# Kernel optimization log

Measured on AMD Instinct MI355X. Metric: run time of the kernel, lower is better.

Reference implementation:

```python
import jax, jax.numpy as jnp
import numpy as np

B, T, HIDDEN, CQ, CKV, NH, HD, RD = 4, 4096, 4096, 1536, 512, 32, 128, 64


def _rope(x):
    # x: (b, s, n, r); positions = arange(s) (decode step gets pos 0, matching
    # the module which passes no offset to RotaryPositionEmbedding)
    s, r = x.shape[1], x.shape[-1]
    inv_freq = 1.0 / (10000.0 ** (jnp.arange(0, r, 2, dtype=jnp.float32) / r))
    ang = jnp.arange(s, dtype=jnp.float32)[:, None] * inv_freq[None, :]  # (s, r/2)
    cos = jnp.cos(ang)[None, :, None, :].astype(x.dtype)
    sin = jnp.sin(ang)[None, :, None, :].astype(x.dtype)
    x1, x2 = x[..., ::2], x[..., 1::2]
    return jnp.stack([x1 * cos - x2 * sin, x1 * sin + x2 * cos], axis=-1).reshape(x.shape)


def setup_inputs() -> dict:
    key = jax.random.key(0)
    ks = jax.random.split(key, 12)
    wscale = jnp.float32(0.02)
    return {
        "hidden_states": jax.random.normal(ks[0], (B, 1, HIDDEN), jnp.float32),
        "mask": jnp.zeros((B, 1, NH, T + 1), jnp.float32),
        "cached_cKV": jax.random.normal(ks[1], (B, T, CKV), jnp.float32),
        "cached_kR": jax.random.normal(ks[2], (B, T, NH, RD), jnp.float32),
        "W_DQ": jax.random.normal(ks[3], (HIDDEN, CQ), jnp.float32) * wscale,
        "W_DKV": jax.random.normal(ks[4], (HIDDEN, CKV), jnp.float32) * wscale,
        "W_UQ_C": jax.random.normal(ks[5], (CQ, NH, HD), jnp.float32) * wscale,
        "W_UQ_R": jax.random.normal(ks[6], (CQ, NH, RD), jnp.float32) * wscale,
        "W_UK_C": jax.random.normal(ks[7], (CKV, NH, HD), jnp.float32) * wscale,
        "W_UV_C": jax.random.normal(ks[8], (CKV, NH, HD), jnp.float32) * wscale,
        "W_KR": jax.random.normal(ks[9], (HIDDEN, NH, RD), jnp.float32) * wscale,
        "W_O": jax.random.normal(ks[10], (NH, HD, HIDDEN), jnp.float32) * wscale,
    }


def reference(hidden_states, mask, cached_cKV, cached_kR,
              W_DQ, W_DKV, W_UQ_C, W_UQ_R, W_UK_C, W_UV_C, W_KR, W_O):
    Bc = hidden_states.shape[0]
    # query path
    cQ_t = jnp.einsum('bsh,hq->bsq', hidden_states, W_DQ)
    qC_t = jnp.einsum('bsq,qnd->bsnd', cQ_t, W_UQ_C)
    qR_t = jnp.einsum('bsq,qnr->bsnr', cQ_t, W_UQ_R)
    kR_t_raw = jnp.einsum('bsh,hnr->bsnr', hidden_states, W_KR)
    qR_t = _rope(qR_t)
    kR_t = _rope(kR_t_raw)
    # compressed KV for the new token
    cKV_t = jnp.einsum('bsh,hv->bsv', hidden_states, W_DKV)
    kC_t = jnp.einsum('bsv,vnd->bsnd', cKV_t, W_UK_C)
    vC_t = jnp.einsum('bsv,vnd->bsnd', cKV_t, W_UV_C)
    # decompress prefix cache and score
    prefix_len = cached_cKV.shape[1]
    kC_prefix = jnp.einsum('btv,vnd->btnd', cached_cKV, W_UK_C)   # (B,T,n,d)
    prefix_scores = (jnp.einsum('bsnd,btnd->bsnt', qC_t, kC_prefix)
                     + jnp.einsum('bsnr,btnr->bsnt', qR_t, cached_kR))
    new_score = (jnp.einsum('bsnd,bsnd->bsn', qC_t, kC_t)
                 + jnp.einsum('bsnr,bsnr->bsn', qR_t, kR_t))[..., None]
    attn_scores = jnp.concatenate([prefix_scores, new_score], axis=-1)
    scale = jnp.sqrt(jnp.float32(HD + RD)).astype(attn_scores.dtype)
    attn_scores = attn_scores / scale
    if mask is not None:
        attn_scores = attn_scores + mask * jnp.asarray(-1e9, attn_scores.dtype)
    attn_probs = jax.nn.softmax(attn_scores, axis=-1)
    # value aggregation
    vC_prefix = jnp.einsum('btv,vnd->btnd', cached_cKV, W_UV_C)
    prefix_agg = jnp.einsum('bsnt,btnd->bsnd', attn_probs[..., :prefix_len], vC_prefix)
    new_agg = attn_probs[..., -1:].reshape(Bc, 1, NH, 1) * vC_t
    attn_out = prefix_agg + new_agg
    output = jnp.einsum('bsnd,ndh->bsh', attn_out, W_O)
    new_cached_cKV = jnp.concatenate([cached_cKV, cKV_t], axis=1)
    new_cached_kR = jnp.concatenate([cached_kR, kR_t], axis=1)
    return (output, new_cached_cKV, new_cached_kR)
```

## Files before the change

### kernel.cpp

```cpp
#include <hip/hip_runtime.h>

#define TT 4096
#define T1 4097

using f32x4 = __attribute__((ext_vector_type(4))) float;

__device__ __forceinline__ void gemv_body(const float* __restrict__ X,
                                          const float* __restrict__ W,
                                          float* __restrict__ Y,
                                          int N, int K, int chunk, int ky) {
  const int tid = threadIdx.x;
  const int ct = tid & 7;
  const int kt = tid >> 3;
  const int col0 = blockIdx.x * 32 + ct * 4;
  const int k0 = ky * chunk;
  float acc[4][4];
#pragma unroll
  for (int c = 0; c < 4; ++c)
#pragma unroll
    for (int b = 0; b < 4; ++b) acc[c][b] = 0.f;
  const int iters = chunk >> 5;
  for (int i = 0; i < iters; ++i) {
    int k = k0 + kt + (i << 5);
    f32x4 w4 = *(const f32x4*)(W + (size_t)k * N + col0);
    float xb[4];
#pragma unroll
    for (int b = 0; b < 4; ++b) xb[b] = X[(size_t)b * K + k];
#pragma unroll
    for (int c = 0; c < 4; ++c)
#pragma unroll
      for (int b = 0; b < 4; ++b) acc[c][b] += w4[c] * xb[b];
  }
  __shared__ float red[256][16];
#pragma unroll
  for (int c = 0; c < 4; ++c)
#pragma unroll
    for (int b = 0; b < 4; ++b) red[tid][c * 4 + b] = acc[c][b];
  __syncthreads();
  for (int s = 16; s >= 1; s >>= 1) {
    if (kt < s) {
#pragma unroll
      for (int j = 0; j < 16; ++j) red[tid][j] += red[tid + 8 * s][j];
    }
    __syncthreads();
  }
  if (kt == 0) {
#pragma unroll
    for (int c = 0; c < 4; ++c)
#pragma unroll
      for (int b = 0; b < 4; ++b)
        atomicAdd(&Y[(size_t)b * N + col0 + c], red[ct][c * 4 + b]);
  }
}

__global__ __launch_bounds__(256) void gemv_hidden(const float* __restrict__ X,
                                                   const float* __restrict__ W0,
                                                   const float* __restrict__ W1,
                                                   const float* __restrict__ W2,
                                                   float* __restrict__ Ybase) {
  const int z = blockIdx.z;
  const float* W = (z == 0) ? W0 : (z == 1) ? W1 : W2;
  const int N = (z == 0) ? 1536 : (z == 1) ? 512 : 2048;
  const int nb = (z == 0) ? 48 : (z == 1) ? 16 : 64;
  const size_t yoff = (z == 0) ? 0 : (z == 1) ? 6144 : 8192;
  if ((int)blockIdx.x >= nb) return;
  gemv_body(X, W, Ybase + yoff, N, 4096, 512, blockIdx.y);
}

__global__ __launch_bounds__(256) void gemv_cq(const float* __restrict__ X,
                                               const float* __restrict__ W0,
                                               const float* __restrict__ W1,
                                               float* __restrict__ Y0,
                                               float* __restrict__ Y1) {
  const int z = blockIdx.z;
  const float* W = (z == 0) ? W0 : W1;
  float* Y = (z == 0) ? Y0 : Y1;
  const int N = (z == 0) ? 4096 : 2048;
  const int nb = (z == 0) ? 128 : 64;
  if ((int)blockIdx.x >= nb) return;
  gemv_body(X, W, Y, N, 1536, 384, blockIdx.y);
}

__global__ __launch_bounds__(256) void gemv_atomic(const float* __restrict__ X,
                                                   const float* __restrict__ W,
                                                   float* __restrict__ Y,
                                                   int N, int K, int chunk) {
  gemv_body(X, W, Y, N, K, chunk, blockIdx.y);
}

__global__ __launch_bounds__(128) void absorb_kernel(const float* __restrict__ qC,
                                                     const float* __restrict__ W_UK,
                                                     float* __restrict__ q_abs,
                                                     float* __restrict__ qT) {
  const int n = blockIdx.x, vt = blockIdx.y;
  __shared__ float qs[4][128];
  for (int i = threadIdx.x; i < 512; i += 128)
    qs[i >> 7][i & 127] = qC[(size_t)(i >> 7) * 4096 + n * 128 + (i & 127)];
  __syncthreads();
  const int v = vt * 128 + threadIdx.x;
  const float* wp = W_UK + (size_t)v * 4096 + n * 128;
  float acc[4] = {0.f, 0.f, 0.f, 0.f};
#pragma unroll 8
  for (int c = 0; c < 32; ++c) {
    f32x4 w4 = *(const f32x4*)(wp + c * 4);
#pragma unroll
    for (int j = 0; j < 4; ++j)
#pragma unroll
      for (int b = 0; b < 4; ++b) acc[b] += qs[b][c * 4 + j] * w4[j];
  }
#pragma unroll
  for (int b = 0; b < 4; ++b) {
    q_abs[((size_t)(b * 32) + n) * 512 + v] = acc[b];
    qT[((size_t)b * 512 + v) * 32 + n] = acc[b];
  }
}

__global__ __launch_bounds__(256, 4) void scores_split(const float* __restrict__ cKV,
                                                       const float* __restrict__ kR,
                                                       const float* __restrict__ qT,
                                                       const float* __restrict__ qR,
                                                       float* __restrict__ scores,
                                                       float* __restrict__ scoresR,
                                                       float* __restrict__ out_ckv,
                                                       float* __restrict__ out_kr) {
  const int bid = blockIdx.x;
  const int idx = bid >> 1;
  const int tid = threadIdx.x;
  const int b = idx >> 9;
  const int t0 = (idx & 511) * 8;
  __shared__ float ck[8][516];
  if (bid & 1) {
    for (int i = tid; i < 1024; i += 256) {
      int tl = i >> 7, vq = i & 127;
      f32x4 v = *(const f32x4*)(cKV + ((size_t)b * TT + t0 + tl) * 512 + vq * 4);
      *(f32x4*)&ck[tl][vq * 4] = v;
      __builtin_nontemporal_store(v, (f32x4*)(out_ckv + ((size_t)b * T1 + t0 + tl) * 512 + vq * 4));
    }
    __syncthreads();
    const int tl = tid >> 5, n = tid & 31;
    const float* qtb = qT + (size_t)b * 16384 + n;
    float a = 0.f;
#pragma unroll 8
    for (int v = 0; v < 512; ++v) a += qtb[(size_t)v * 32] * ck[tl][v];
    scores[((size_t)(b * 32) + n) * T1 + t0 + tl] = a;
  } else {
    const int w = tid >> 6, l = tid & 63;
    f32x4 q[8];
#pragma unroll
    for (int k = 0; k < 8; ++k)
      q[k] = *(const f32x4*)(qR + (size_t)b * 2048 + l * 4 + k * 256);
    const int nbase = l >> 4;
    const int wlead = ((l & 15) == 0);
#pragma unroll
    for (int r = 0; r < 2; ++r) {
      const int t = t0 + w * 2 + r;
      const float* src = kR + ((size_t)b * TT + t) * 2048 + l * 4;
      float* dst = out_kr + ((size_t)b * T1 + t) * 2048 + l * 4;
      f32x4 v[8];
#pragma unroll
      for (int k = 0; k < 8; ++k) v[k] = *(const f32x4*)(src + k * 256);
#pragma unroll
      for (int k = 0; k < 8; ++k)
        __builtin_nontemporal_store(v[k], (f32x4*)(dst + k * 256));
      float p[8];
#pragma unroll
      for (int k = 0; k < 8; ++k)
        p[k] = (q[k][0] * v[k][0] + q[k][1] * v[k][1]) +
               (q[k][2] * v[k][2] + q[k][3] * v[k][3]);
#pragma unroll
      for (int k = 0; k < 8; ++k) {
        p[k] += __shfl_xor(p[k], 1);
        p[k] += __shfl_xor(p[k], 2);
        p[k] += __shfl_xor(p[k], 4);
        p[k] += __shfl_xor(p[k], 8);
      }
      if (wlead) {
#pragma unroll
        for (int k = 0; k < 8; ++k)
          scoresR[((size_t)(b * 32) + k * 4 + nbase) * T1 + t] = p[k];
      }
    }
  }
}

__global__ __launch_bounds__(256) void softmax_stats(const float* __restrict__ scores,
                                                     const float* __restrict__ scoresR,
                                                     const float* __restrict__ mask,
                                                     const float* __restrict__ q_abs,
                                                     const float* __restrict__ cKV_t,
                                                     const float* __restrict__ qR,
                                                     const float* __restrict__ kR_t,
                                                     float* __restrict__ stats) {
  const int b = blockIdx.x >> 5, n = blockIdx.x & 31;
  const int tid = threadIdx.x;
  const size_t row = (size_t)(b * 32) + n;
  const float* srow = scores + row * T1;
  const float* scrow = scoresR + row * T1;
  const float* mrow = mask + row * T1;
  const float* qa = q_abs + row * 512;
  const float* ck = cKV_t + b * 512;
  float p = qa[tid] * ck[tid] + qa[tid + 256] * ck[tid + 256];
  if (tid < 64) p += qR[(size_t)b * 2048 + n * 64 + tid] * kR_t[(size_t)b * 2048 + n * 64 + tid];
  __shared__ float lds[256];
  lds[tid] = p;
  __syncthreads();
  for (int s = 128; s >= 1; s >>= 1) {
    if (tid < s) lds[tid] += lds[tid + s];
    __syncthreads();
  }
  const float sT = lds[0];
  __syncthreads();
  const float isc = 0.0721687836487032f;
  float m = -1e30f, s = 0.f;
  for (int t = tid; t < TT; t += 256) {
    float val = (srow[t] + scrow[t]) * isc + mrow[t] * (-1e9f);
    if (val > m) {
      s = s * expf(m - val) + 1.f;
      m = val;
    } else {
      s += expf(val - m);
    }
  }
  __shared__ float lm[256], lsm[256];
  lm[tid] = m;
  lsm[tid] = s;
  __syncthreads();
  for (int st = 128; st >= 1; st >>= 1) {
    if (tid < st) {
      float m2 = lm[tid + st], s2 = lsm[tid + st];
      float M = fmaxf(lm[tid], m2);
      lsm[tid] = lsm[tid] * expf(lm[tid] - M) + s2 * expf(m2 - M);
      lm[tid] = M;
    }
    __syncthreads();
  }
  if (tid == 0) {
    float valT = sT * isc + mrow[TT] * (-1e9f);
    float M = fmaxf(lm[0], valT);
    float S = lsm[0] * expf(lm[0] - M) + expf(valT - M);
    stats[blockIdx.x * 4 + 0] = M;
    stats[blockIdx.x * 4 + 1] = 1.f / S;
    stats[blockIdx.x * 4 + 2] = expf(valT - M) / S;
  }
}

__global__ __launch_bounds__(256) void agg_part(const float* __restrict__ cKV,
                                                const float* __restrict__ scores,
                                                const float* __restrict__ scoresR,
                                                const float* __restrict__ mask,
                                                const float* __restrict__ stats,
                                                float* __restrict__ aggP,
                                                int tlen, int NC) {
  const int chunk = blockIdx.x, b = blockIdx.y, vh = blockIdx.z;
  const int tid = threadIdx.x;
  const int vg = tid & 31, ng = tid >> 5;
  const float isc = 0.0721687836487032f;
  __shared__ float p_lds[32 * 129];
  float acc[4][4];
#pragma unroll
  for (int a = 0; a < 4; ++a)
#pragma unroll
    for (int j = 0; j < 4; ++j) acc[a][j] = 0.f;
  const int sub = (tlen < 128) ? tlen : 128;
  const int sshift = (sub == 64) ? 6 : 7;
  for (int tt = 0; tt < tlen; tt += sub) {
    const int t0 = chunk * tlen + tt;
    __syncthreads();
    for (int i = tid; i < (sub << 5); i += 256) {
      int nn = i >> sshift, tl = i & (sub - 1);
      size_t row = (size_t)(b * 32) + nn;
      size_t off = row * T1 + t0 + tl;
      float val = (scores[off] + scoresR[off]) * isc + mask[off] * (-1e9f);
      p_lds[nn * 129 + tl] = expf(val - stats[row * 4]) * stats[row * 4 + 1];
    }
    __syncthreads();
    const float* cbase = cKV + ((size_t)b * TT + t0) * 512 + vh * 128 + vg * 4;
    for (int t = 0; t < sub; t += 2) {
      f32x4 c0 = *(const f32x4*)(cbase + (size_t)t * 512);
      f32x4 c1 = *(const f32x4*)(cbase + (size_t)(t + 1) * 512);
#pragma unroll
      for (int a = 0; a < 4; ++a) {
        float p0 = p_lds[(ng * 4 + a) * 129 + t];
        float p1 = p_lds[(ng * 4 + a) * 129 + t + 1];
#pragma unroll
        for (int j = 0; j < 4; ++j) acc[a][j] += p0 * c0[j] + p1 * c1[j];
      }
    }
  }
#pragma unroll
  for (int a = 0; a < 4; ++a) {
    int n = ng * 4 + a;
    float* dst = aggP + (((size_t)b * NC + chunk) * 32 + n) * 512 + vh * 128 + vg * 4;
    f32x4 v;
#pragma unroll
    for (int j = 0; j < 4; ++j) v[j] = acc[a][j];
    *(f32x4*)dst = v;
  }
}

__global__ __launch_bounds__(256) void agg_reduce(const float* __restrict__ aggP,
                                                  const float* __restrict__ stats,
                                                  const float* __restrict__ cKV_t,
                                                  float* __restrict__ agg, int NC) {
  const int idx = blockIdx.x * 256 + threadIdx.x;
  const int b = idx >> 14;
  const int n = (idx >> 9) & 31;
  const int v = idx & 511;
  float s = stats[((size_t)(b * 32) + n) * 4 + 2] * cKV_t[b * 512 + v];
  const float* pp = aggP + (((size_t)b * NC) * 32 + n) * 512 + v;
#pragma unroll 4
  for (int c = 0; c < NC; ++c) s += pp[(size_t)c * 32 * 512];
  agg[idx] = s;
}

__global__ __launch_bounds__(256) void out1_kernel(const float* __restrict__ agg,
                                                   const float* __restrict__ W_UV,
                                                   float* __restrict__ attn_out) {
  const int n = blockIdx.x, vc = blockIdx.y;
  const int tid = threadIdx.x;
  const int d = tid & 127, bh = tid >> 7;
  const float* a0 = agg + ((size_t)(bh * 32) + n) * 512;
  const float* a1 = agg + ((size_t)((bh + 2) * 32) + n) * 512;
  float acc0 = 0.f, acc1 = 0.f;
#pragma unroll 4
  for (int vv = 0; vv < 64; ++vv) {
    int v = vc * 64 + vv;
    float w = W_UV[(size_t)v * 4096 + n * 128 + d];
    acc0 += a0[v] * w;
    acc1 += a1[v] * w;
  }
  atomicAdd(&attn_out[(size_t)bh * 4096 + n * 128 + d], acc0);
  atomicAdd(&attn_out[(size_t)(bh + 2) * 4096 + n * 128 + d], acc1);
}

__global__ __launch_bounds__(256) void finalize_kernel(const float* __restrict__ outf,
                                                       const float* __restrict__ cKV_t,
                                                       const float* __restrict__ kR_t,
                                                       float* __restrict__ out) {
  int idx = blockIdx.x * 256 + threadIdx.x;
  if (idx < 16384) {
    out[idx] = outf[idx];
    return;
  }
  idx -= 16384;
  if (idx < 2048) {
    int b = idx >> 9, v = idx & 511;
    out[16384 + ((size_t)b * T1 + TT) * 512 + v] = cKV_t[idx];
    return;
  }
  idx -= 2048;
  if (idx < 8192) {
    int b = idx >> 11;
    int c = idx & 2047;
    out[16384 + (size_t)8390656 + ((size_t)b * T1 + TT) * 2048 + c] = kR_t[idx];
  }
}

extern "C" void kernel_launch(void* const* d_in, const int* in_sizes, int n_in,
                              void* d_out, int out_size, void* d_ws, size_t ws_size,
                              hipStream_t stream) {
  (void)in_sizes; (void)n_in; (void)out_size;
  const float* hidden = (const float*)d_in[0];
  const float* mask   = (const float*)d_in[1];
  const float* cKV    = (const float*)d_in[2];
  const float* kR     = (const float*)d_in[3];
  const float* W_DQ   = (const float*)d_in[4];
  const float* W_DKV  = (const float*)d_in[5];
  const float* W_UQ_C = (const float*)d_in[6];
  const float* W_UQ_R = (const float*)d_in[7];
  const float* W_UK_C = (const float*)d_in[8];
  const float* W_UV_C = (const float*)d_in[9];
  const float* W_KR   = (const float*)d_in[10];
  const float* W_O    = (const float*)d_in[11];

  float* ws = (float*)d_ws;
  const size_t WS_CQ = 0;
  const size_t WS_CKVT = 6144;
  const size_t WS_KRT = 8192;
  const size_t WS_QC = 16384;
  const size_t WS_QR = 32768;
  const size_t WS_OUTF = 40960;
  const size_t WS_ATTN = 57344;
  const size_t WS_STATS = 73728;
  const size_t WS_AGG = 74240;
  const size_t WS_QABS = 139776;
  const size_t WS_QT = 205312;
  const size_t WS_SCORES = 270848;
  const size_t WS_SCR = 795264;
  const size_t WS_AGGP = 1319680;

  int NC = 8;
  if (ws_size >= (WS_AGGP + (size_t)64 * 65536) * 4) NC = 64;
  else if (ws_size >= (WS_AGGP + (size_t)32 * 65536) * 4) NC = 32;
  else if (ws_size >= (WS_AGGP + (size_t)16 * 65536) * 4) NC = 16;
  const int tlen = 4096 / NC;

  float* out0 = (float*)d_out;
  float* out_ckv = out0 + 16384;
  float* out_kr = out_ckv + (size_t)8390656;

  hipMemsetAsync(d_ws, 0, 73728 * sizeof(float), stream);

  gemv_hidden<<<dim3(64, 8, 3), 256, 0, stream>>>(hidden, W_DQ, W_DKV, W_KR, ws);
  gemv_cq<<<dim3(128, 4, 2), 256, 0, stream>>>(ws + WS_CQ, W_UQ_C, W_UQ_R,
                                               ws + WS_QC, ws + WS_QR);
  absorb_kernel<<<dim3(32, 4), 128, 0, stream>>>(ws + WS_QC, W_UK_C, ws + WS_QABS, ws + WS_QT);
  scores_split<<<4096, 256, 0, stream>>>(cKV, kR, ws + WS_QT, ws + WS_QR,
                                         ws + WS_SCORES, ws + WS_SCR, out_ckv, out_kr);
  softmax_stats<<<128, 256, 0, stream>>>(ws + WS_SCORES, ws + WS_SCR, mask, ws + WS_QABS,
                                         ws + WS_CKVT, ws + WS_QR, ws + WS_KRT, ws + WS_STATS);
  agg_part<<<dim3(NC, 4, 4), 256, 0, stream>>>(cKV, ws + WS_SCORES, ws + WS_SCR, mask,
                                               ws + WS_STATS, ws + WS_AGGP, tlen, NC);
  agg_reduce<<<256, 256, 0, stream>>>(ws + WS_AGGP, ws + WS_STATS, ws + WS_CKVT,
                                      ws + WS_AGG, NC);
  out1_kernel<<<dim3(32, 8), 256, 0, stream>>>(ws + WS_AGG, W_UV_C, ws + WS_ATTN);
  gemv_atomic<<<dim3(128, 8), 256, 0, stream>>>(ws + WS_ATTN, W_O, ws + WS_OUTF, 4096, 4096, 512);
  finalize_kernel<<<104, 256, 0, stream>>>(ws + WS_OUTF, ws + WS_CKVT, ws + WS_KRT, out0);
}
```

Baseline: 199.6 us.

## Fuse softmax statistics into aggregation with flash-style online rescaling per chunk

Removes the separate softmax_stats pass over the score rows. agg_part now computes a running max and sum per head and chunk, rescaling its accumulators as it goes. A small stats_merge kernel then combines the per-chunk statistics with the new-token score into scale factors, which agg_reduce applies when summing the chunk partials. This saves one full read of the scores, scoresR and mask arrays and one kernel launch. In exchange it adds reductions, extra barriers and exp work inside agg_part, plus two tiny kernels, and it switches to the faster, less accurate __expf.

```diff
diff --git a/kernel.cpp b/kernel.cpp
--- a/kernel.cpp
+++ b/kernel.cpp
@@ -113,6 +113,27 @@
     q_abs[((size_t)(b * 32) + n) * 512 + v] = acc[b];
     qT[((size_t)b * 512 + v) * 32 + n] = acc[b];
   }
+}
+
+__global__ __launch_bounds__(64) void newtok_kernel(const float* __restrict__ q_abs,
+                                                    const float* __restrict__ cKV_t,
+                                                    const float* __restrict__ qR,
+                                                    const float* __restrict__ kR_t,
+                                                    const float* __restrict__ mask,
+                                                    float* __restrict__ valT) {
+  const int row = blockIdx.x;
+  const int b = row >> 5, n = row & 31;
+  const int l = threadIdx.x;
+  const float* qa = q_abs + (size_t)row * 512;
+  const float* ck = cKV_t + b * 512;
+  float p = 0.f;
+#pragma unroll
+  for (int j = 0; j < 8; ++j) p += qa[l + 64 * j] * ck[l + 64 * j];
+  p += qR[(size_t)b * 2048 + n * 64 + l] * kR_t[(size_t)b * 2048 + n * 64 + l];
+#pragma unroll
+  for (int s = 1; s < 64; s <<= 1) p += __shfl_xor(p, s);
+  if (l == 0)
+    valT[row] = p * 0.0721687836487032f + mask[(size_t)row * T1 + TT] * (-1e9f);
 }
 
 __global__ __launch_bounds__(256, 4) void scores_split(const float* __restrict__ cKV,
@@ -183,79 +204,20 @@
   }
 }
 
-__global__ __launch_bounds__(256) void softmax_stats(const float* __restrict__ scores,
-                                                     const float* __restrict__ scoresR,
-                                                     const float* __restrict__ mask,
-                                                     const float* __restrict__ q_abs,
-                                                     const float* __restrict__ cKV_t,
-                                                     const float* __restrict__ qR,
-                                                     const float* __restrict__ kR_t,
-                                                     float* __restrict__ stats) {
-  const int b = blockIdx.x >> 5, n = blockIdx.x & 31;
-  const int tid = threadIdx.x;
-  const size_t row = (size_t)(b * 32) + n;
-  const float* srow = scores + row * T1;
-  const float* scrow = scoresR + row * T1;
-  const float* mrow = mask + row * T1;
-  const float* qa = q_abs + row * 512;
-  const float* ck = cKV_t + b * 512;
-  float p = qa[tid] * ck[tid] + qa[tid + 256] * ck[tid + 256];
-  if (tid < 64) p += qR[(size_t)b * 2048 + n * 64 + tid] * kR_t[(size_t)b * 2048 + n * 64 + tid];
-  __shared__ float lds[256];
-  lds[tid] = p;
-  __syncthreads();
-  for (int s = 128; s >= 1; s >>= 1) {
-    if (tid < s) lds[tid] += lds[tid + s];
-    __syncthreads();
-  }
-  const float sT = lds[0];
-  __syncthreads();
-  const float isc = 0.0721687836487032f;
-  float m = -1e30f, s = 0.f;
-  for (int t = tid; t < TT; t += 256) {
-    float val = (srow[t] + scrow[t]) * isc + mrow[t] * (-1e9f);
-    if (val > m) {
-      s = s * expf(m - val) + 1.f;
-      m = val;
-    } else {
-      s += expf(val - m);
-    }
-  }
-  __shared__ float lm[256], lsm[256];
-  lm[tid] = m;
-  lsm[tid] = s;
-  __syncthreads();
-  for (int st = 128; st >= 1; st >>= 1) {
-    if (tid < st) {
-      float m2 = lm[tid + st], s2 = lsm[tid + st];
-      float M = fmaxf(lm[tid], m2);
-      lsm[tid] = lsm[tid] * expf(lm[tid] - M) + s2 * expf(m2 - M);
-      lm[tid] = M;
-    }
-    __syncthreads();
-  }
-  if (tid == 0) {
-    float valT = sT * isc + mrow[TT] * (-1e9f);
-    float M = fmaxf(lm[0], valT);
-    float S = lsm[0] * expf(lm[0] - M) + expf(valT - M);
-    stats[blockIdx.x * 4 + 0] = M;
-    stats[blockIdx.x * 4 + 1] = 1.f / S;
-    stats[blockIdx.x * 4 + 2] = expf(valT - M) / S;
-  }
-}
-
 __global__ __launch_bounds__(256) void agg_part(const float* __restrict__ cKV,
                                                 const float* __restrict__ scores,
                                                 const float* __restrict__ scoresR,
                                                 const float* __restrict__ mask,
-                                                const float* __restrict__ stats,
                                                 float* __restrict__ aggP,
+                                                float* __restrict__ statsC,
                                                 int tlen, int NC) {
   const int chunk = blockIdx.x, b = blockIdx.y, vh = blockIdx.z;
   const int tid = threadIdx.x;
   const int vg = tid & 31, ng = tid >> 5;
   const float isc = 0.0721687836487032f;
   __shared__ float p_lds[32 * 129];
+  __shared__ float gm[32], gs[32], scl[32];
+  if (tid < 32) { gm[tid] = -1e30f; gs[tid] = 0.f; }
   float acc[4][4];
 #pragma unroll
   for (int a = 0; a < 4; ++a)
@@ -270,10 +232,45 @@
       int nn = i >> sshift, tl = i & (sub - 1);
       size_t row = (size_t)(b * 32) + nn;
       size_t off = row * T1 + t0 + tl;
-      float val = (scores[off] + scoresR[off]) * isc + mask[off] * (-1e9f);
-      p_lds[nn * 129 + tl] = expf(val - stats[row * 4]) * stats[row * 4 + 1];
-    }
-    __syncthreads();
+      p_lds[nn * 129 + tl] = (scores[off] + scoresR[off]) * isc + mask[off] * (-1e9f);
+    }
+    __syncthreads();
+    {
+      const int n8 = tid >> 3, lane = tid & 7;
+      float mx = -1e30f;
+      for (int t = lane; t < sub; t += 8) mx = fmaxf(mx, p_lds[n8 * 129 + t]);
+      mx = fmaxf(mx, __shfl_xor(mx, 1));
+      mx = fmaxf(mx, __shfl_xor(mx, 2));
+      mx = fmaxf(mx, __shfl_xor(mx, 4));
+      if (lane == 0) {
+        float newM = fmaxf(gm[n8], mx);
+        float sc = __expf(gm[n8] - newM);
+        scl[n8] = sc;
+        gm[n8] = newM;
+        gs[n8] *= sc;
+      }
+    }
+    __syncthreads();
+#pragma unroll
+    for (int a = 0; a < 4; ++a) {
+      float sc = scl[ng * 4 + a];
+#pragma unroll
+      for (int j = 0; j < 4; ++j) acc[a][j] *= sc;
+    }
+    for (int i = tid; i < (sub << 5); i += 256) {
+      int nn = i >> sshift, tl = i & (sub - 1);
+      p_lds[nn * 129 + tl] = __expf(p_lds[nn * 129 + tl] - gm[nn]);
+    }
+    __syncthreads();
+    {
+      const int n8 = tid >> 3, lane = tid & 7;
+      float se = 0.f;
+      for (int t = lane; t < sub; t += 8) se += p_lds[n8 * 129 + t];
+      se += __shfl_xor(se, 1);
+      se += __shfl_xor(se, 2);
+      se += __shfl_xor(se, 4);
+      if (lane == 0) gs[n8] += se;
+    }
     const float* cbase = cKV + ((size_t)b * TT + t0) * 512 + vh * 128 + vg * 4;
     for (int t = 0; t < sub; t += 2) {
       f32x4 c0 = *(const f32x4*)(cbase + (size_t)t * 512);
@@ -287,6 +284,7 @@
       }
     }
   }
+  __syncthreads();
 #pragma unroll
   for (int a = 0; a < 4; ++a) {
     int n = ng * 4 + a;
@@ -296,20 +294,53 @@
     for (int j = 0; j < 4; ++j) v[j] = acc[a][j];
     *(f32x4*)dst = v;
   }
+  if (vh == 0 && tid < 32) {
+    size_t o = ((size_t)(b * 32) + tid) * NC + chunk;
+    statsC[2 * o] = gm[tid];
+    statsC[2 * o + 1] = gs[tid];
+  }
+}
+
+__global__ __launch_bounds__(64) void stats_merge(const float* __restrict__ statsC,
+                                                  const float* __restrict__ valT,
+                                                  float* __restrict__ fact,
+                                                  float* __restrict__ fT, int NC) {
+  const int row = blockIdx.x;
+  const int l = threadIdx.x;
+  const float vt = valT[row];
+  float mc = -1e30f, sc = 0.f;
+  if (l < NC) {
+    mc = statsC[2 * ((size_t)row * NC + l)];
+    sc = statsC[2 * ((size_t)row * NC + l) + 1];
+  }
+  float m = fmaxf(mc, vt);
+#pragma unroll
+  for (int s = 1; s < 64; s <<= 1) m = fmaxf(m, __shfl_xor(m, s));
+  float e = (l < NC) ? sc * __expf(mc - m) : 0.f;
+  float S = e;
+#pragma unroll
+  for (int s = 1; s < 64; s <<= 1) S += __shfl_xor(S, s);
+  S += __expf(vt - m);
+  const float invS = 1.0f / S;
+  if (l < NC) fact[(size_t)row * NC + l] = __expf(mc - m) * invS;
+  if (l == 0) fT[row] = __expf(vt - m) * invS;
 }
 
 __global__ __launch_bounds__(256) void agg_reduce(const float* __restrict__ aggP,
-                                                  const float* __restrict__ stats,
+                                                  const float* __restrict__ fact,
+                                                  const float* __restrict__ fT,
                                                   const float* __restrict__ cKV_t,
                                                   float* __restrict__ agg, int NC) {
   const int idx = blockIdx.x * 256 + threadIdx.x;
   const int b = idx >> 14;
   const int n = (idx >> 9) & 31;
   const int v = idx & 511;
-  float s = stats[((size_t)(b * 32) + n) * 4 + 2] * cKV_t[b * 512 + v];
+  const size_t row = (size_t)(b * 32) + n;
+  float s = fT[row] * cKV_t[b * 512 + v];
   const float* pp = aggP + (((size_t)b * NC) * 32 + n) * 512 + v;
+  const float* fc = fact + row * NC;
 #pragma unroll 4
-  for (int c = 0; c < NC; ++c) s += pp[(size_t)c * 32 * 512];
+  for (int c = 0; c < NC; ++c) s += pp[(size_t)c * 32 * 512] * fc[c];
   agg[idx] = s;
 }
 
@@ -381,13 +412,16 @@
   const size_t WS_QR = 32768;
   const size_t WS_OUTF = 40960;
   const size_t WS_ATTN = 57344;
-  const size_t WS_STATS = 73728;
+  const size_t WS_VALT = 73728;
   const size_t WS_AGG = 74240;
   const size_t WS_QABS = 139776;
   const size_t WS_QT = 205312;
   const size_t WS_SCORES = 270848;
   const size_t WS_SCR = 795264;
-  const size_t WS_AGGP = 1319680;
+  const size_t WS_STATSC = 1319680;
+  const size_t WS_FACT = 1336064;
+  const size_t WS_FT = 1344256;
+  const size_t WS_AGGP = 1344512;
 
   int NC = 8;
   if (ws_size >= (WS_AGGP + (size_t)64 * 65536) * 4) NC = 64;
@@ -405,14 +439,16 @@
   gemv_cq<<<dim3(128, 4, 2), 256, 0, stream>>>(ws + WS_CQ, W_UQ_C, W_UQ_R,
                                                ws + WS_QC, ws + WS_QR);
   absorb_kernel<<<dim3(32, 4), 128, 0, stream>>>(ws + WS_QC, W_UK_C, ws + WS_QABS, ws + WS_QT);
+  newtok_kernel<<<128, 64, 0, stream>>>(ws + WS_QABS, ws + WS_CKVT, ws + WS_QR,
+                                        ws + WS_KRT, mask, ws + WS_VALT);
   scores_split<<<4096, 256, 0, stream>>>(cKV, kR, ws + WS_QT, ws + WS_QR,
                                          ws + WS_SCORES, ws + WS_SCR, out_ckv, out_kr);
-  softmax_stats<<<128, 256, 0, stream>>>(ws + WS_SCORES, ws + WS_SCR, mask, ws + WS_QABS,
-                                         ws + WS_CKVT, ws + WS_QR, ws + WS_KRT, ws + WS_STATS);
   agg_part<<<dim3(NC, 4, 4), 256, 0, stream>>>(cKV, ws + WS_SCORES, ws + WS_SCR, mask,
-                                               ws + WS_STATS, ws + WS_AGGP, tlen, NC);
-  agg_reduce<<<256, 256, 0, stream>>>(ws + WS_AGGP, ws + WS_STATS, ws + WS_CKVT,
-                                      ws + WS_AGG, NC);
+                                               ws + WS_AGGP, ws + WS_STATSC, tlen, NC);
+  stats_merge<<<128, 64, 0, stream>>>(ws + WS_STATSC, ws + WS_VALT, ws + WS_FACT,
+                                      ws + WS_FT, NC);
+  agg_reduce<<<256, 256, 0, stream>>>(ws + WS_AGGP, ws + WS_FACT, ws + WS_FT,
+                                      ws + WS_CKVT, ws + WS_AGG, NC);
   out1_kernel<<<dim3(32, 8), 256, 0, stream>>>(ws + WS_AGG, W_UV_C, ws + WS_ATTN);
   gemv_atomic<<<dim3(128, 8), 256, 0, stream>>>(ws + WS_ATTN, W_O, ws + WS_OUTF, 4096, 4096, 512);
   finalize_kernel<<<104, 256, 0, stream>>>(ws + WS_OUTF, ws + WS_CKVT, ws + WS_KRT, out0);
```

Measured after the change: 194.9 us (median of 2 runs). 2.3% less time.
